# Kernel optimization log

Hardware: AMD Instinct MI355X
Metric: run time of the kernel (lower is better)

## Reference

```python
import jax, jax.numpy as jnp
import numpy as np

NEG_SLOPE = 0.2  # PyG GATConv default
LN_EPS = 1e-5

B, N, DIN, H, DH, DOUT = 256, 256, 128, 4, 32, 1


def setup_inputs() -> dict:
    key = jax.random.key(0)
    ks = jax.random.split(key, 12)
    s = lambda *shape: 0.1
    return {
        "x": jax.random.normal(ks[0], (B, N, DIN), jnp.float32),
        "adj": jnp.ones((B, N, N), jnp.float32),  # unused (graph is fully connected)
        # GATConv 1: dim_in -> H heads x DH
        "W1": jax.random.normal(ks[1], (DIN, H * DH), jnp.float32) * 0.05,
        "b1": jnp.zeros((H * DH,), jnp.float32),
        "att_src1": jax.random.normal(ks[2], (H, DH), jnp.float32) * 0.1,
        "att_dst1": jax.random.normal(ks[3], (H, DH), jnp.float32) * 0.1,
        # LayerNorm over hidden dim H*DH
        "gamma": jnp.ones((H * DH,), jnp.float32),
        "beta": jnp.zeros((H * DH,), jnp.float32),
        # GATConv 2: H*DH -> 1 head x DOUT, concat=False
        "W2": jax.random.normal(ks[4], (H * DH, DOUT), jnp.float32) * 0.05,
        "b2": jnp.zeros((DOUT,), jnp.float32),
        "att_src2": jax.random.normal(ks[5], (1, DOUT), jnp.float32) * 0.1,
        "att_dst2": jax.random.normal(ks[6], (1, DOUT), jnp.float32) * 0.1,
    }


def _gat_layer(x, W, b, att_src, att_dst):
    """Dense GATConv on a fully-connected graph.
    x: [B, N, Fin] -> out: [B, N, H, D], attn: [B, H, N, N].
    Node i aggregates over all j: e_ij = leaky_relu(a_dst.h_i + a_src.h_j).
    """
    Hh, D = att_src.shape
    h = (x @ W).reshape(x.shape[0], x.shape[1], Hh, D)          # [B,N,H,D]
    a_src = jnp.einsum("bnhd,hd->bnh", h, att_src)              # neighbor term
    a_dst = jnp.einsum("bnhd,hd->bnh", h, att_dst)              # central term
    e = a_dst.transpose(0, 2, 1)[:, :, :, None] + a_src.transpose(0, 2, 1)[:, :, None, :]  # [B,H,N,N]
    e = jax.nn.leaky_relu(e, NEG_SLOPE)
    attn = jax.nn.softmax(e, axis=-1)                           # softmax over neighbors j
    out = jnp.einsum("bhij,bjhd->bihd", attn, h)                # [B,N,H,D]
    return out, attn, b


def reference(x, adj, W1, b1, att_src1, att_dst1, gamma, beta, W2, b2, att_src2, att_dst2):
    del adj  # module ignores adj; graph is fully connected
    # layer 1: concat heads
    h1, _, _ = _gat_layer(x, W1, b1, att_src1, att_dst1)
    h1 = h1.reshape(B, N, H * DH) + b1                          # [B,N,H*DH]
    # LayerNorm over hidden dim
    mu = jnp.mean(h1, axis=-1, keepdims=True)
    var = jnp.mean(jnp.square(h1 - mu), axis=-1, keepdims=True)
    h1 = (h1 - mu) * jax.lax.rsqrt(var + LN_EPS) * gamma + beta
    # layer 2: single head, concat=False (mean over 1 head == identity)
    h2, attn2, _ = _gat_layer(h1, W2, b2, att_src2, att_dst2)
    h2 = h2.reshape(B, N, DOUT) + b2
    out = jax.nn.elu(h2)                                        # [B,N,DOUT]
    return out
```

## Files before the change

kernel.cpp:

```cpp
#include <hip/hip_runtime.h>
#include <hip/hip_bf16.h>
#include <math.h>

#define BB 256
#define NN 256
#define DIN 128
#define NH 4
#define DH 32
#define HID 128
#define NEG 0.2f
#define LN_EPS 1e-5f

typedef __hip_bfloat16 bf16;
typedef __attribute__((ext_vector_type(8))) short short8;
typedef __attribute__((ext_vector_type(4))) short short4v;
typedef __attribute__((ext_vector_type(4))) float float4v;

__device__ __forceinline__ float s2f(short s) {
    return __uint_as_float(((unsigned int)(unsigned short)s) << 16);
}
__device__ __forceinline__ short f2bs(float f) { return (short)__bfloat16_as_ushort(__float2bfloat16(f)); }
__device__ __forceinline__ float lrelu(float x) { return fmaxf(x, NEG * x); }

#define MFMA16(a, b, c) __builtin_amdgcn_mfma_f32_16x16x32_bf16(a, b, c, 0, 0, 0)

__global__ __launch_bounds__(256) void k_prep(const float* __restrict__ W1,
                                              short* __restrict__ W1T) {
    const int idx = blockIdx.x * 256 + threadIdx.x;
    const int n = idx >> 7, k = idx & 127;
    W1T[idx] = f2bs(W1[k * HID + n]);
}

__global__ __launch_bounds__(512) void k_mega(
    const float* __restrict__ x, const short* __restrict__ W1T,
    const float* __restrict__ as1, const float* __restrict__ ad1,
    const float* __restrict__ b1, const float* __restrict__ gamma,
    const float* __restrict__ beta, const float* __restrict__ W2,
    const float* __restrict__ bias2, const float* __restrict__ att_src2,
    const float* __restrict__ att_dst2, float* __restrict__ out)
{
    const int b = blockIdx.x, t = threadIdx.x;
    const int w = t >> 6, lane = t & 63;
    const int l16 = lane & 15, q = lane >> 4;

    __shared__ short uA[34816];
    __shared__ short haggT[128 * 268];
    __shared__ float ss[4][256], dd[4][256];
    __shared__ float b1s[HID], gws[HID], bws[HID], atts[HID], attd[HID];
    __shared__ float smaxs[4], Ssc[2];
    __shared__ float h2v[NN], svv[NN];

    const float* xb = x + (size_t)b * NN * DIN;
#pragma unroll
    for (int it = 0; it < 16; ++it) {
        const int idx = t + it * 512;
        const int row = idx >> 5, c4 = idx & 31;
        const float4v v = ((const float4v*)xb)[idx];
        short4v p;
        p[0] = f2bs(v[0]); p[1] = f2bs(v[1]); p[2] = f2bs(v[2]); p[3] = f2bs(v[3]);
        *(short4v*)&uA[row * 136 + c4 * 4] = p;
    }
    if (t < HID) {
        b1s[t] = b1[t];
        const float w2v = W2[t];
        gws[t] = gamma[t] * w2v;
        bws[t] = beta[t] * w2v;
        atts[t] = as1[t];
        attd[t] = ad1[t];
    }
    __syncthreads();

    float4v acc1[16];
#pragma unroll
    for (int i = 0; i < 16; ++i) acc1[i] = (float4v){0.f, 0.f, 0.f, 0.f};
    const short* w1row = W1T + (w * 16 + l16) * DIN;
#pragma unroll
    for (int ks = 0; ks < 4; ++ks) {
        const short8 afr = *(const short8*)(w1row + ks * 32 + q * 8);
#pragma unroll
        for (int nt = 0; nt < 16; ++nt) {
            const short8 bfr = *(const short8*)&uA[(nt * 16 + l16) * 136 + ks * 32 + q * 8];
            acc1[nt] = MFMA16(afr, bfr, acc1[nt]);
        }
    }
    __syncthreads();

#pragma unroll
    for (int nt = 0; nt < 16; ++nt)
#pragma unroll
        for (int r = 0; r < 4; ++r)
            uA[(w * 16 + q * 4 + r) * 272 + nt * 16 + l16] = f2bs(acc1[nt][r]);
    __syncthreads();

#pragma unroll
    for (int rep = 0; rep < 2; ++rep) {
        const int id = t + rep * 512;
        const int hh = id >> 8, j = id & 255;
        float vs = 0.f, vd = 0.f;
#pragma unroll 8
        for (int d2 = 0; d2 < 32; ++d2) {
            const float hv = s2f(uA[(hh * 32 + d2) * 272 + j]);
            vs = fmaf(hv, atts[hh * 32 + d2], vs);
            vd = fmaf(hv, attd[hh * 32 + d2], vd);
        }
        ss[hh][j] = vs;
        dd[hh][j] = vd;
    }
    __syncthreads();

    if (w < 4) {
        float mv = fmaxf(fmaxf(ss[w][lane], ss[w][lane + 64]),
                         fmaxf(ss[w][lane + 128], ss[w][lane + 192]));
#pragma unroll
        for (int m = 1; m < 64; m <<= 1) mv = fmaxf(mv, __shfl_xor(mv, m, 64));
        if (lane == 0) smaxs[w] = mv;
    } else if (w == 4 || w == 5) {
        const float* src = (w == 4) ? gws : bws;
        float v = src[lane] + src[lane + 64];
#pragma unroll
        for (int m = 1; m < 64; m <<= 1) v += __shfl_xor(v, m, 64);
        if (lane == 0) Ssc[w - 4] = v;
    }
    __syncthreads();

    const int hh = w >> 1, half = w & 1;
    const float smax = smaxs[hh];
    float dI[8], mI[8], lI[8];
#pragma unroll
    for (int u = 0; u < 8; ++u) {
        const int i = half * 128 + u * 16 + l16;
        dI[u] = dd[hh][i];
        mI[u] = lrelu(dI[u] + smax);
        lI[u] = 0.f;
    }
    float4v acc2[8][2];
#pragma unroll
    for (int u = 0; u < 8; ++u) {
        acc2[u][0] = (float4v){0.f, 0.f, 0.f, 0.f};
        acc2[u][1] = (float4v){0.f, 0.f, 0.f, 0.f};
    }
    const short* hTh = &uA[(hh * 32) * 272];
#pragma unroll 2
    for (int ks = 0; ks < 8; ++ks) {
        const short8 a0 = *(const short8*)&hTh[l16 * 272 + ks * 32 + q * 8];
        const short8 a1 = *(const short8*)&hTh[(16 + l16) * 272 + ks * 32 + q * 8];
        const float4v s0 = *(const float4v*)&ss[hh][ks * 32 + q * 8];
        const float4v s1 = *(const float4v*)&ss[hh][ks * 32 + q * 8 + 4];
        const float sj[8] = {s0[0], s0[1], s0[2], s0[3], s1[0], s1[1], s1[2], s1[3]};
#pragma unroll
        for (int u = 0; u < 8; ++u) {
            short8 bfr;
            float ls = lI[u];
#pragma unroll
            for (int jj = 0; jj < 8; ++jj) {
                float e = dI[u] + sj[jj];
                e = fmaxf(e, NEG * e);
                const float wgt = __expf(e - mI[u]);
                ls += wgt;
                bfr[jj] = f2bs(wgt);
            }
            lI[u] = ls;
            acc2[u][0] = MFMA16(a0, bfr, acc2[u][0]);
            acc2[u][1] = MFMA16(a1, bfr, acc2[u][1]);
        }
    }
#pragma unroll
    for (int u = 0; u < 8; ++u) {
        float l = lI[u];
        l += __shfl_xor(l, 16, 64);
        l += __shfl_xor(l, 32, 64);
        const float inv = 1.f / l;
        const int i = half * 128 + u * 16 + l16;
#pragma unroll
        for (int mt = 0; mt < 2; ++mt)
#pragma unroll
            for (int r = 0; r < 4; ++r)
                haggT[(hh * 32 + mt * 16 + q * 4 + r) * 268 + i] = f2bs(acc2[u][mt][r] * inv);
    }
    __syncthreads();

    float* pp3 = &dd[0][0];
    const int i3 = t & 255, hf = t >> 8;
    {
        float s = 0.f, sq = 0.f, t3 = 0.f;
#pragma unroll 8
        for (int dz = 0; dz < 64; ++dz) {
            const int d = hf * 64 + dz;
            const float v = s2f(haggT[d * 268 + i3]) + b1s[d];
            s += v;
            sq = fmaf(v, v, sq);
            t3 = fmaf(v, gws[d], t3);
        }
        if (hf) { pp3[i3 * 3] = s; pp3[i3 * 3 + 1] = sq; pp3[i3 * 3 + 2] = t3; }
        __syncthreads();
        if (!hf) {
            s += pp3[i3 * 3]; sq += pp3[i3 * 3 + 1]; t3 += pp3[i3 * 3 + 2];
            const float mu = s * (1.f / HID);
            const float var = sq * (1.f / HID) - mu * mu;
            const float rs = rsqrtf(var + LN_EPS);
            const float h2 = rs * (t3 - mu * Ssc[0]) + Ssc[1];
            h2v[i3] = h2;
            svv[i3] = h2 * att_src2[0];
        }
    }
    __syncthreads();

    float* pq = &ss[0][0];
    const float d_att = att_dst2[0];
    const float di = h2v[i3] * d_att;
    float mloc = -1e30f;
#pragma unroll 4
    for (int jz = 0; jz < 128; ++jz)
        mloc = fmaxf(mloc, lrelu(di + svv[hf * 128 + jz]));
    if (hf) pp3[i3] = mloc;
    __syncthreads();
    if (!hf) pp3[i3] = fmaxf(mloc, pp3[i3]);
    __syncthreads();
    const float mfin = pp3[i3];
    float l2 = 0.f, num = 0.f;
#pragma unroll 4
    for (int jz = 0; jz < 128; ++jz) {
        const int j = hf * 128 + jz;
        const float wgt = __expf(lrelu(di + svv[j]) - mfin);
        l2 += wgt;
        num = fmaf(wgt, h2v[j], num);
    }
    if (hf) { pq[i3 * 2] = l2; pq[i3 * 2 + 1] = num; }
    __syncthreads();
    if (!hf) {
        l2 += pq[i3 * 2];
        num += pq[i3 * 2 + 1];
        float o = num / l2 + bias2[0];
        o = (o > 0.f) ? o : (__expf(o) - 1.f);
        out[b * NN + i3] = o;
    }
}

extern "C" void kernel_launch(void* const* d_in, const int* in_sizes, int n_in,
                              void* d_out, int out_size, void* d_ws, size_t ws_size,
                              hipStream_t stream) {
    const float* x   = (const float*)d_in[0];
    const float* W1  = (const float*)d_in[2];
    const float* b1  = (const float*)d_in[3];
    const float* as1 = (const float*)d_in[4];
    const float* ad1 = (const float*)d_in[5];
    const float* gam = (const float*)d_in[6];
    const float* bet = (const float*)d_in[7];
    const float* W2  = (const float*)d_in[8];
    const float* bi2 = (const float*)d_in[9];
    const float* as2 = (const float*)d_in[10];
    const float* ad2 = (const float*)d_in[11];
    float* out = (float*)d_out;

    short* W1T = (short*)d_ws;

    k_prep<<<DIN * HID / 256, 256, 0, stream>>>(W1, W1T);
    k_mega<<<BB, 512, 0, stream>>>(x, W1T, as1, ad1, b1, gam, bet, W2,
                                   bi2, as2, ad2, out);
}
```

Before: 163.7 us.

## Fold W1 transpose into mega kernel and double block to 1024 threads

Removes the separate W1 prep kernel: each block loads and transposes W1 into shared memory itself. The fused kernel now runs 1024 threads per block, and every stage is re-split across 16 waves (GEMM tiles, attention quarters, 4-way partial reductions for LayerNorm and layer 2). It also replaces the library bf16 conversion with a cheaper round-half-up bit trick that packs two values at once. The aim is to cut launch overhead and raise per-block parallelism. The costs are redundant W1 loading in every block, more shared-memory reduction traffic, and slightly different rounding (no NaN handling).

Measured after the change: 163.0 us. No clear change (-0.4%).

```diff
diff --git a/kernel.cpp b/kernel.cpp
--- a/kernel.cpp
+++ b/kernel.cpp
@@ -13,26 +13,25 @@
 
 typedef __hip_bfloat16 bf16;
 typedef __attribute__((ext_vector_type(8))) short short8;
-typedef __attribute__((ext_vector_type(4))) short short4v;
 typedef __attribute__((ext_vector_type(4))) float float4v;
+typedef __attribute__((ext_vector_type(2))) unsigned int uint2v;
 
 __device__ __forceinline__ float s2f(short s) {
     return __uint_as_float(((unsigned int)(unsigned short)s) << 16);
 }
-__device__ __forceinline__ short f2bs(float f) { return (short)__bfloat16_as_ushort(__float2bfloat16(f)); }
+__device__ __forceinline__ short f2bs(float f) {
+    return (short)((__float_as_uint(f) + 0x8000u) >> 16);
+}
+__device__ __forceinline__ unsigned int pack2(float a, float b) {
+    return ((__float_as_uint(a) + 0x8000u) >> 16) |
+           ((__float_as_uint(b) + 0x8000u) & 0xffff0000u);
+}
 __device__ __forceinline__ float lrelu(float x) { return fmaxf(x, NEG * x); }
 
 #define MFMA16(a, b, c) __builtin_amdgcn_mfma_f32_16x16x32_bf16(a, b, c, 0, 0, 0)
 
-__global__ __launch_bounds__(256) void k_prep(const float* __restrict__ W1,
-                                              short* __restrict__ W1T) {
-    const int idx = blockIdx.x * 256 + threadIdx.x;
-    const int n = idx >> 7, k = idx & 127;
-    W1T[idx] = f2bs(W1[k * HID + n]);
-}
-
-__global__ __launch_bounds__(512) void k_mega(
-    const float* __restrict__ x, const short* __restrict__ W1T,
+__global__ __launch_bounds__(1024) void k_mega(
+    const float* __restrict__ x, const float* __restrict__ W1,
     const float* __restrict__ as1, const float* __restrict__ ad1,
     const float* __restrict__ b1, const float* __restrict__ gamma,
     const float* __restrict__ beta, const float* __restrict__ W2,
@@ -44,21 +43,31 @@
     const int l16 = lane & 15, q = lane >> 4;
 
     __shared__ short uA[34816];
-    __shared__ short haggT[128 * 268];
-    __shared__ float ss[4][256], dd[4][256];
+    __shared__ short hR[34816];
+    __shared__ float ss[NH][NN], dd[NH][NN];
     __shared__ float b1s[HID], gws[HID], bws[HID], atts[HID], attd[HID];
-    __shared__ float smaxs[4], Ssc[2];
+    __shared__ float smaxs[NH], Ssc[2];
     __shared__ float h2v[NN], svv[NN];
 
     const float* xb = x + (size_t)b * NN * DIN;
 #pragma unroll
-    for (int it = 0; it < 16; ++it) {
-        const int idx = t + it * 512;
+    for (int it = 0; it < 8; ++it) {
+        const int idx = t + it * 1024;
         const int row = idx >> 5, c4 = idx & 31;
         const float4v v = ((const float4v*)xb)[idx];
-        short4v p;
-        p[0] = f2bs(v[0]); p[1] = f2bs(v[1]); p[2] = f2bs(v[2]); p[3] = f2bs(v[3]);
-        *(short4v*)&uA[row * 136 + c4 * 4] = p;
+        uint2v p;
+        p[0] = pack2(v[0], v[1]);
+        p[1] = pack2(v[2], v[3]);
+        *(uint2v*)&uA[row * 136 + c4 * 4] = p;
+    }
+#pragma unroll
+    for (int it = 0; it < 4; ++it) {
+        const int idx = t + it * 1024;
+        const int k = idx >> 5, n4 = idx & 31;
+        const float4v v = ((const float4v*)W1)[idx];
+#pragma unroll
+        for (int e = 0; e < 4; ++e)
+            hR[(n4 * 4 + e) * 136 + k] = f2bs(v[e]);
     }
     if (t < HID) {
         b1s[t] = b1[t];
@@ -70,41 +79,39 @@
     }
     __syncthreads();
 
-    float4v acc1[16];
-#pragma unroll
-    for (int i = 0; i < 16; ++i) acc1[i] = (float4v){0.f, 0.f, 0.f, 0.f};
-    const short* w1row = W1T + (w * 16 + l16) * DIN;
+    const int dtile = w & 7, jhalf = w >> 3;
+    float4v acc1[8];
+#pragma unroll
+    for (int i = 0; i < 8; ++i) acc1[i] = (float4v){0.f, 0.f, 0.f, 0.f};
+    const short* arow = &hR[(dtile * 16 + l16) * 136];
 #pragma unroll
     for (int ks = 0; ks < 4; ++ks) {
-        const short8 afr = *(const short8*)(w1row + ks * 32 + q * 8);
-#pragma unroll
-        for (int nt = 0; nt < 16; ++nt) {
-            const short8 bfr = *(const short8*)&uA[(nt * 16 + l16) * 136 + ks * 32 + q * 8];
+        const short8 afr = *(const short8*)&arow[ks * 32 + q * 8];
+#pragma unroll
+        for (int nt = 0; nt < 8; ++nt) {
+            const short8 bfr = *(const short8*)&uA[((jhalf * 8 + nt) * 16 + l16) * 136 + ks * 32 + q * 8];
             acc1[nt] = MFMA16(afr, bfr, acc1[nt]);
         }
     }
     __syncthreads();
-
-#pragma unroll
-    for (int nt = 0; nt < 16; ++nt)
+#pragma unroll
+    for (int nt = 0; nt < 8; ++nt)
 #pragma unroll
         for (int r = 0; r < 4; ++r)
-            uA[(w * 16 + q * 4 + r) * 272 + nt * 16 + l16] = f2bs(acc1[nt][r]);
-    __syncthreads();
-
-#pragma unroll
-    for (int rep = 0; rep < 2; ++rep) {
-        const int id = t + rep * 512;
-        const int hh = id >> 8, j = id & 255;
+            uA[(dtile * 16 + q * 4 + r) * 272 + (jhalf * 8 + nt) * 16 + l16] = f2bs(acc1[nt][r]);
+    __syncthreads();
+
+    {
+        const int hs = t >> 8, js = t & 255;
         float vs = 0.f, vd = 0.f;
 #pragma unroll 8
         for (int d2 = 0; d2 < 32; ++d2) {
-            const float hv = s2f(uA[(hh * 32 + d2) * 272 + j]);
-            vs = fmaf(hv, atts[hh * 32 + d2], vs);
-            vd = fmaf(hv, attd[hh * 32 + d2], vd);
-        }
-        ss[hh][j] = vs;
-        dd[hh][j] = vd;
+            const float hv = s2f(uA[(hs * 32 + d2) * 272 + js]);
+            vs = fmaf(hv, atts[hs * 32 + d2], vs);
+            vd = fmaf(hv, attd[hs * 32 + d2], vd);
+        }
+        ss[hs][js] = vs;
+        dd[hs][js] = vd;
     }
     __syncthreads();
 
@@ -123,78 +130,87 @@
     }
     __syncthreads();
 
-    const int hh = w >> 1, half = w & 1;
-    const float smax = smaxs[hh];
-    float dI[8], mI[8], lI[8];
-#pragma unroll
-    for (int u = 0; u < 8; ++u) {
-        const int i = half * 128 + u * 16 + l16;
-        dI[u] = dd[hh][i];
-        mI[u] = lrelu(dI[u] + smax);
-        lI[u] = 0.f;
-    }
-    float4v acc2[8][2];
-#pragma unroll
-    for (int u = 0; u < 8; ++u) {
-        acc2[u][0] = (float4v){0.f, 0.f, 0.f, 0.f};
-        acc2[u][1] = (float4v){0.f, 0.f, 0.f, 0.f};
-    }
-    const short* hTh = &uA[(hh * 32) * 272];
+    {
+        const int hh = w >> 2, qtr = w & 3;
+        const float smax = smaxs[hh];
+        float dI[4], mI[4], lI[4];
+#pragma unroll
+        for (int u = 0; u < 4; ++u) {
+            const int i = qtr * 64 + u * 16 + l16;
+            dI[u] = dd[hh][i];
+            mI[u] = lrelu(dI[u] + smax);
+            lI[u] = 0.f;
+        }
+        float4v acc2[4][2];
+#pragma unroll
+        for (int u = 0; u < 4; ++u) {
+            acc2[u][0] = (float4v){0.f, 0.f, 0.f, 0.f};
+            acc2[u][1] = (float4v){0.f, 0.f, 0.f, 0.f};
+        }
+        const short* hTh = &uA[(hh * 32) * 272];
 #pragma unroll 2
-    for (int ks = 0; ks < 8; ++ks) {
-        const short8 a0 = *(const short8*)&hTh[l16 * 272 + ks * 32 + q * 8];
-        const short8 a1 = *(const short8*)&hTh[(16 + l16) * 272 + ks * 32 + q * 8];
-        const float4v s0 = *(const float4v*)&ss[hh][ks * 32 + q * 8];
-        const float4v s1 = *(const float4v*)&ss[hh][ks * 32 + q * 8 + 4];
-        const float sj[8] = {s0[0], s0[1], s0[2], s0[3], s1[0], s1[1], s1[2], s1[3]};
-#pragma unroll
-        for (int u = 0; u < 8; ++u) {
-            short8 bfr;
-            float ls = lI[u];
-#pragma unroll
-            for (int jj = 0; jj < 8; ++jj) {
-                float e = dI[u] + sj[jj];
-                e = fmaxf(e, NEG * e);
-                const float wgt = __expf(e - mI[u]);
-                ls += wgt;
-                bfr[jj] = f2bs(wgt);
+        for (int ks = 0; ks < 8; ++ks) {
+            const short8 a0 = *(const short8*)&hTh[l16 * 272 + ks * 32 + q * 8];
+            const short8 a1 = *(const short8*)&hTh[(16 + l16) * 272 + ks * 32 + q * 8];
+            const float4v s0 = *(const float4v*)&ss[hh][ks * 32 + q * 8];
+            const float4v s1 = *(const float4v*)&ss[hh][ks * 32 + q * 8 + 4];
+            const float sj[8] = {s0[0], s0[1], s0[2], s0[3], s1[0], s1[1], s1[2], s1[3]};
+#pragma unroll
+            for (int u = 0; u < 4; ++u) {
+                union { short8 s8; unsigned int u32[4]; } bfr;
+                float ls = lI[u];
+#pragma unroll
+                for (int p = 0; p < 4; ++p) {
+                    float e0 = dI[u] + sj[2 * p];
+                    float e1 = dI[u] + sj[2 * p + 1];
+                    e0 = fmaxf(e0, NEG * e0);
+                    e1 = fmaxf(e1, NEG * e1);
+                    const float w0 = __expf(e0 - mI[u]);
+                    const float w1 = __expf(e1 - mI[u]);
+                    ls += w0 + w1;
+                    bfr.u32[p] = pack2(w0, w1);
+                }
+                lI[u] = ls;
+                acc2[u][0] = MFMA16(a0, bfr.s8, acc2[u][0]);
+                acc2[u][1] = MFMA16(a1, bfr.s8, acc2[u][1]);
             }
-            lI[u] = ls;
-            acc2[u][0] = MFMA16(a0, bfr, acc2[u][0]);
-            acc2[u][1] = MFMA16(a1, bfr, acc2[u][1]);
-        }
-    }
-#pragma unroll
-    for (int u = 0; u < 8; ++u) {
-        float l = lI[u];
-        l += __shfl_xor(l, 16, 64);
-        l += __shfl_xor(l, 32, 64);
-        const float inv = 1.f / l;
-        const int i = half * 128 + u * 16 + l16;
-#pragma unroll
-        for (int mt = 0; mt < 2; ++mt)
-#pragma unroll
-            for (int r = 0; r < 4; ++r)
-                haggT[(hh * 32 + mt * 16 + q * 4 + r) * 268 + i] = f2bs(acc2[u][mt][r] * inv);
-    }
-    __syncthreads();
-
-    float* pp3 = &dd[0][0];
+        }
+#pragma unroll
+        for (int u = 0; u < 4; ++u) {
+            float l = lI[u];
+            l += __shfl_xor(l, 16, 64);
+            l += __shfl_xor(l, 32, 64);
+            const float inv = 1.f / l;
+            const int i = qtr * 64 + u * 16 + l16;
+#pragma unroll
+            for (int mt = 0; mt < 2; ++mt)
+#pragma unroll
+                for (int r = 0; r < 4; ++r)
+                    hR[(hh * 32 + mt * 16 + q * 4 + r) * 272 + i] = f2bs(acc2[u][mt][r] * inv);
+        }
+    }
+    __syncthreads();
+
+    float* pw = (float*)uA;
     const int i3 = t & 255, hf = t >> 8;
     {
         float s = 0.f, sq = 0.f, t3 = 0.f;
 #pragma unroll 8
-        for (int dz = 0; dz < 64; ++dz) {
-            const int d = hf * 64 + dz;
-            const float v = s2f(haggT[d * 268 + i3]) + b1s[d];
+        for (int dz = 0; dz < 32; ++dz) {
+            const int d = hf * 32 + dz;
+            const float v = s2f(hR[d * 272 + i3]) + b1s[d];
             s += v;
             sq = fmaf(v, v, sq);
             t3 = fmaf(v, gws[d], t3);
         }
-        if (hf) { pp3[i3 * 3] = s; pp3[i3 * 3 + 1] = sq; pp3[i3 * 3 + 2] = t3; }
+        const int pbase = (hf * 256 + i3) * 3;
+        pw[pbase] = s; pw[pbase + 1] = sq; pw[pbase + 2] = t3;
         __syncthreads();
-        if (!hf) {
-            s += pp3[i3 * 3]; sq += pp3[i3 * 3 + 1]; t3 += pp3[i3 * 3 + 2];
+        if (hf == 0) {
+            for (int k = 1; k < 4; ++k) {
+                const int pb = (k * 256 + i3) * 3;
+                s += pw[pb]; sq += pw[pb + 1]; t3 += pw[pb + 2];
+            }
             const float mu = s * (1.f / HID);
             const float var = sq * (1.f / HID) - mu * mu;
             const float rs = rsqrtf(var + LN_EPS);
@@ -205,34 +221,38 @@
     }
     __syncthreads();
 
-    float* pq = &ss[0][0];
-    const float d_att = att_dst2[0];
-    const float di = h2v[i3] * d_att;
-    float mloc = -1e30f;
+    {
+        const float di = h2v[i3] * att_dst2[0];
+        float mloc = -1e30f;
 #pragma unroll 4
-    for (int jz = 0; jz < 128; ++jz)
-        mloc = fmaxf(mloc, lrelu(di + svv[hf * 128 + jz]));
-    if (hf) pp3[i3] = mloc;
-    __syncthreads();
-    if (!hf) pp3[i3] = fmaxf(mloc, pp3[i3]);
-    __syncthreads();
-    const float mfin = pp3[i3];
-    float l2 = 0.f, num = 0.f;
+        for (int jz = 0; jz < 64; ++jz)
+            mloc = fmaxf(mloc, lrelu(di + svv[hf * 64 + jz]));
+        pw[4096 + hf * 256 + i3] = mloc;
+        __syncthreads();
+        float mfin = pw[4096 + i3];
+#pragma unroll
+        for (int k = 1; k < 4; ++k) mfin = fmaxf(mfin, pw[4096 + k * 256 + i3]);
+        float l2 = 0.f, num = 0.f;
 #pragma unroll 4
-    for (int jz = 0; jz < 128; ++jz) {
-        const int j = hf * 128 + jz;
-        const float wgt = __expf(lrelu(di + svv[j]) - mfin);
-        l2 += wgt;
-        num = fmaf(wgt, h2v[j], num);
-    }
-    if (hf) { pq[i3 * 2] = l2; pq[i3 * 2 + 1] = num; }
-    __syncthreads();
-    if (!hf) {
-        l2 += pq[i3 * 2];
-        num += pq[i3 * 2 + 1];
-        float o = num / l2 + bias2[0];
-        o = (o > 0.f) ? o : (__expf(o) - 1.f);
-        out[b * NN + i3] = o;
+        for (int jz = 0; jz < 64; ++jz) {
+            const int j = hf * 64 + jz;
+            const float wgt = __expf(lrelu(di + svv[j]) - mfin);
+            l2 += wgt;
+            num = fmaf(wgt, h2v[j], num);
+        }
+        const int qb = 5120 + (hf * 256 + i3) * 2;
+        pw[qb] = l2; pw[qb + 1] = num;
+        __syncthreads();
+        if (hf == 0) {
+#pragma unroll
+            for (int k = 1; k < 4; ++k) {
+                const int pb = 5120 + (k * 256 + i3) * 2;
+                l2 += pw[pb]; num += pw[pb + 1];
+            }
+            float o = num / l2 + bias2[0];
+            o = (o > 0.f) ? o : (__expf(o) - 1.f);
+            out[b * NN + i3] = o;
+        }
     }
 }
 
@@ -252,9 +272,6 @@
     const float* ad2 = (const float*)d_in[11];
     float* out = (float*)d_out;
 
-    short* W1T = (short*)d_ws;
-
-    k_prep<<<DIN * HID / 256, 256, 0, stream>>>(W1, W1T);
-    k_mega<<<BB, 512, 0, stream>>>(x, W1T, as1, ad1, b1, gam, bet, W2,
-                                   bi2, as2, ad2, out);
-}
+    k_mega<<<BB, 1024, 0, stream>>>(x, W1, as1, ad1, b1, gam, bet, W2,
+                                    bi2, as2, ad2, out);
+}
```
